# Kernel optimization log

Hardware: AMD Instinct MI355X
Metric: run time of the kernel (lower is better)

The kernel has to match this reference:

```python
import jax, jax.numpy as jnp
import numpy as np

T, B_SZ = 1024, 1024
NX, NU, ND, NM, NDT, NH = 128, 64, 32, 32, 32, 128


def setup_inputs() -> dict:
    key = jax.random.key(0)
    ks = jax.random.split(key, 10)
    return {
        "x": jax.random.normal(ks[0], (B_SZ, NX), jnp.float32),
        "M_flow": jax.random.normal(ks[1], (T, B_SZ, NM), jnp.float32),
        "DT": jax.random.normal(ks[2], (T, B_SZ, NDT), jnp.float32),
        "D": jax.random.normal(ks[3], (T, B_SZ, ND), jnp.float32),
        # ConstrainedLinear(nx, nx): weight and scalar init with torch.rand -> uniform[0,1)
        "A_weight": jax.random.uniform(ks[4], (NX, NX), jnp.float32),
        "A_scalar": jax.random.uniform(ks[5], (NX, NX), jnp.float32),
        # nn.Linear(in, out, bias=False) weights are [out, in]
        "B_w": jax.random.normal(ks[6], (NX, NU), jnp.float32) * (1.0 / np.sqrt(NU)),
        "E_w": jax.random.normal(ks[7], (NX, ND), jnp.float32) * (1.0 / np.sqrt(ND)),
        "hf1_w": jax.random.normal(ks[8], (NH, NM + NDT), jnp.float32) * (1.0 / np.sqrt(NM + NDT)),
        "hf2_w": jax.random.normal(ks[9], (NU, NH), jnp.float32) * (1.0 / np.sqrt(NH)),
    }


def reference(x, M_flow, DT, D, A_weight, A_scalar, B_w, E_w, hf1_w, hf2_w):
    # Constrained weight: ((1 - 0.1*sigmoid(scalar)) * softmax(weight, dim=1)).T
    # It is constant across time, so compute once (torch redundantly recomputes it per step).
    s_clamped = 1.0 - 0.1 * jax.nn.sigmoid(A_scalar)
    W_eff = (s_clamped * jax.nn.softmax(A_weight, axis=1)).T  # [nx, nx]

    # Per-step control input u_t depends only on exogenous M_flow/DT -> vectorize over time.
    md = jnp.concatenate([M_flow, DT], axis=2)                # [T, B, n_m+n_dT]
    h = jax.nn.relu(jnp.einsum('tbi,hi->tbh', md, hf1_w))     # [T, B, n_hidden]
    u = jax.nn.relu(jnp.einsum('tbh,uh->tbu', h, hf2_w))      # [T, B, nu]

    # Precompute additive drive B(u_t) + E(d_t); only x@W_eff is sequential.
    drive = jnp.einsum('tbu,xu->tbx', u, B_w) + jnp.einsum('tbd,xd->tbx', D, E_w)

    def step(x_prev, drive_t):
        x_new = x_prev @ W_eff + drive_t
        return x_new, x_new

    _, X = jax.lax.scan(step, x, drive)  # X: [T, B, nx]
    Y = X[:, :, -1]                      # [T, B]
    return X, Y
```

## Files before the change

### kernel.cpp

```cpp
#include <hip/hip_runtime.h>

typedef _Float16 h4 __attribute__((ext_vector_type(4)));
typedef _Float16 h8 __attribute__((ext_vector_type(8)));
typedef float f4 __attribute__((ext_vector_type(4)));

#define MFMA16(a, b, c) __builtin_amdgcn_mfma_f32_16x16x32_f16((a), (b), (c), 0, 0, 0)

static constexpr int TT  = 1024;
static constexpr int BS  = 1024;
static constexpr int LCH = 32;
static constexpr int NCH = 32;
static constexpr size_t XTOT = (size_t)TT * BS * 128;

static constexpr size_t WS_WT16 = 0;
static constexpr size_t WS_HF1  = 32768;
static constexpr size_t WS_HF2  = 49152;
static constexpr size_t WS_BW   = 65536;
static constexpr size_t WS_EW   = 81920;
static constexpr size_t WS_W32  = 90112;
static constexpr size_t WS_F    = 131072;
static constexpr size_t WS_INIT = WS_F + (size_t)NCH * BS * 128 * 4;
static constexpr size_t WS_DRV  = WS_INIT + (size_t)NCH * BS * 128 * 4;

template <typename T>
__device__ inline T ntload(const T* p) { return __builtin_nontemporal_load(p); }

__global__ void prep_kernel(const float* __restrict__ Aw, const float* __restrict__ As,
                            const float* __restrict__ hf1, const float* __restrict__ hf2,
                            const float* __restrict__ Bw, const float* __restrict__ Ew,
                            char* __restrict__ ws)
{
    const int tid = threadIdx.x;
    const int bid = blockIdx.x;
    if (bid < 128) {
        __shared__ float red[128];
        const int n = bid;
        const float a = Aw[n * 128 + tid];
        red[tid] = a;
        __syncthreads();
        for (int s = 64; s > 0; s >>= 1) {
            if (tid < s) red[tid] = fmaxf(red[tid], red[tid + s]);
            __syncthreads();
        }
        const float mx = red[0];
        __syncthreads();
        const float e = expf(a - mx);
        red[tid] = e;
        __syncthreads();
        for (int s = 64; s > 0; s >>= 1) {
            if (tid < s) red[tid] += red[tid + s];
            __syncthreads();
        }
        const float sm  = e / red[0];
        const float asv = As[n * 128 + tid];
        const float sc  = 1.0f - 0.1f * (1.0f / (1.0f + expf(-asv)));
        ((_Float16*)(ws + WS_WT16))[n * 128 + tid] = (_Float16)(sc * sm);
    } else {
        const int b2 = bid - 128;
        for (int i = b2 * 128 + tid; i < 8192; i += 32 * 128) {
            ((_Float16*)(ws + WS_HF1))[i] = (_Float16)hf1[i];
            ((_Float16*)(ws + WS_HF2))[i] = (_Float16)hf2[i];
            ((_Float16*)(ws + WS_BW))[i]  = (_Float16)Bw[i];
            if (i < 4096) ((_Float16*)(ws + WS_EW))[i] = (_Float16)Ew[i];
        }
    }
}

__global__ void w32_kernel(char* __restrict__ ws)
{
    const int tid  = threadIdx.x;
    const int lane = tid & 63;
    const int w    = tid >> 6;
    const int cl   = lane & 15;
    const int gq   = lane >> 4;

    __shared__ __align__(16) _Float16 Ta[128 * 128];
    __shared__ __align__(16) _Float16 Tb[128 * 128];

    const _Float16* Wt16 = (const _Float16*)(ws + WS_WT16);
    for (int i = tid; i < 2048; i += 256)
        *(h8*)&Ta[i * 8] = *(const h8*)&Wt16[i * 8];
    __syncthreads();

    for (int s = 0; s < 5; ++s) {
        const _Float16* src = (s & 1) ? Tb : Ta;
        _Float16* dst       = (s & 1) ? Ta : Tb;
        f4 acc[8][2];
#pragma unroll
        for (int mt = 0; mt < 8; ++mt)
#pragma unroll
            for (int nt = 0; nt < 2; ++nt) acc[mt][nt] = f4{};
#pragma unroll
        for (int kk = 0; kk < 4; ++kk) {
            h8 b0, b1;
#pragma unroll
            for (int j = 0; j < 8; ++j) {
                const int kr = kk * 32 + gq * 8 + j;
                b0[j] = src[kr * 128 + w * 32 + cl];
                b1[j] = src[kr * 128 + w * 32 + 16 + cl];
            }
#pragma unroll
            for (int mt = 0; mt < 8; ++mt) {
                h8 a = *(const h8*)&src[(mt * 16 + cl) * 128 + kk * 32 + gq * 8];
                acc[mt][0] = MFMA16(a, b0, acc[mt][0]);
                acc[mt][1] = MFMA16(a, b1, acc[mt][1]);
            }
        }
        __syncthreads();
#pragma unroll
        for (int mt = 0; mt < 8; ++mt)
#pragma unroll
            for (int nt = 0; nt < 2; ++nt)
#pragma unroll
                for (int r = 0; r < 4; ++r)
                    dst[(mt * 16 + gq * 4 + r) * 128 + w * 32 + nt * 16 + cl] =
                        (_Float16)acc[mt][nt][r];
        __syncthreads();
    }
    _Float16* W32 = (_Float16*)(ws + WS_W32);
    for (int i = tid; i < 2048; i += 256)
        *(h8*)&W32[i * 8] = *(const h8*)&Tb[i * 8];
}

__global__ __launch_bounds__(256, 4)
void drive_kernel(const float* __restrict__ Mfl, const float* __restrict__ DTi,
                  const float* __restrict__ Din, char* __restrict__ ws)
{
    const int tid  = threadIdx.x;
    const int lane = tid & 63;
    const int w    = tid >> 6;
    const int cl   = lane & 15;
    const int gq   = lane >> 4;
    const int bt   = blockIdx.x & 63;
    const int tq   = blockIdx.x >> 6;
    const int b0   = bt * 16;

    const _Float16* Hf1  = (const _Float16*)(ws + WS_HF1);
    const _Float16* Hf2  = (const _Float16*)(ws + WS_HF2);
    const _Float16* Bw16 = (const _Float16*)(ws + WS_BW);
    const _Float16* Ew16 = (const _Float16*)(ws + WS_EW);
    _Float16* Drv        = (_Float16*)(ws + WS_DRV);

    __shared__ __align__(16) _Float16 mds[4][16 * 64];
    __shared__ __align__(16) _Float16 dts[4][16 * 32];
    __shared__ __align__(16) _Float16 hs[4][16 * 128];
    __shared__ __align__(16) _Float16 us[4][16 * 64];

    const int qrow = (tid & 127) >> 3;
    const int qc4  = (tid & 7) * 4;
    f4 pm[4], pd[4];
#pragma unroll
    for (int s = 0; s < 4; ++s) {
        const size_t t  = (size_t)tq * 4 + s;
        const size_t rb = (t * BS + b0 + qrow) * 32 + qc4;
        pm[s] = (tid < 128) ? ntload((const f4*)&Mfl[rb]) : ntload((const f4*)&DTi[rb]);
        if (tid < 128) pd[s] = ntload((const f4*)&Din[rb]);
    }
#pragma unroll
    for (int s = 0; s < 4; ++s) {
        const int col = (tid < 128) ? qc4 : (32 + qc4);
        h4 hv;
#pragma unroll
        for (int j = 0; j < 4; ++j) hv[j] = (_Float16)pm[s][j];
        *(h4*)&mds[s][qrow * 64 + (((col >> 3) ^ (qrow & 7)) * 8) + (col & 7)] = hv;
        if (tid < 128) {
            h4 h2;
#pragma unroll
            for (int j = 0; j < 4; ++j) h2[j] = (_Float16)pd[s][j];
            *(h4*)&dts[s][qrow * 32 + (((qc4 >> 3) ^ (qrow & 3)) * 8) + (qc4 & 7)] = h2;
        }
    }

    h8 hf1f[2][2], bwf[2][2], ewf[2], hf2f[4];
#pragma unroll
    for (int nt = 0; nt < 2; ++nt) {
        const int ng = w * 32 + nt * 16 + cl;
#pragma unroll
        for (int kk = 0; kk < 2; ++kk) {
            hf1f[nt][kk] = *(const h8*)&Hf1[ng * 64 + kk * 32 + gq * 8];
            bwf[nt][kk]  = *(const h8*)&Bw16[ng * 64 + kk * 32 + gq * 8];
        }
        ewf[nt] = *(const h8*)&Ew16[ng * 32 + gq * 8];
    }
    {
        const int ng = w * 16 + cl;
#pragma unroll
        for (int kk = 0; kk < 4; ++kk)
            hf2f[kk] = *(const h8*)&Hf2[ng * 128 + kk * 32 + gq * 8];
    }
    __syncthreads();

#pragma unroll
    for (int s = 0; s < 4; ++s) {
        f4 ha[2] = {};
#pragma unroll
        for (int kk = 0; kk < 2; ++kk) {
            h8 a = *(const h8*)&mds[s][cl * 64 + (((kk * 4 + gq) ^ (cl & 7)) * 8)];
            ha[0] = MFMA16(a, hf1f[0][kk], ha[0]);
            ha[1] = MFMA16(a, hf1f[1][kk], ha[1]);
        }
#pragma unroll
        for (int nt = 0; nt < 2; ++nt) {
            const int colg = w * 32 + nt * 16 + cl;
#pragma unroll
            for (int r = 0; r < 4; ++r) {
                const int row = gq * 4 + r;
                hs[s][row * 128 + (((colg >> 3) ^ (row & 15)) * 8) + (colg & 7)] =
                    (_Float16)fmaxf(ha[nt][r], 0.f);
            }
        }
    }
    __syncthreads();

#pragma unroll
    for (int s = 0; s < 4; ++s) {
        f4 ua = {};
#pragma unroll
        for (int kk = 0; kk < 4; ++kk) {
            h8 a = *(const h8*)&hs[s][cl * 128 + (((kk * 4 + gq) ^ (cl & 15)) * 8)];
            ua = MFMA16(a, hf2f[kk], ua);
        }
        const int colg = w * 16 + cl;
#pragma unroll
        for (int r = 0; r < 4; ++r) {
            const int row = gq * 4 + r;
            us[s][row * 64 + (((colg >> 3) ^ (row & 7)) * 8) + (colg & 7)] =
                (_Float16)fmaxf(ua[r], 0.f);
        }
    }
    __syncthreads();

#pragma unroll
    for (int s = 0; s < 4; ++s) {
        f4 acc[2] = {};
#pragma unroll
        for (int kk = 0; kk < 2; ++kk) {
            h8 a = *(const h8*)&us[s][cl * 64 + (((kk * 4 + gq) ^ (cl & 7)) * 8)];
            acc[0] = MFMA16(a, bwf[0][kk], acc[0]);
            acc[1] = MFMA16(a, bwf[1][kk], acc[1]);
        }
        {
            h8 a = *(const h8*)&dts[s][cl * 32 + ((gq ^ (cl & 3)) * 8)];
            acc[0] = MFMA16(a, ewf[0], acc[0]);
            acc[1] = MFMA16(a, ewf[1], acc[1]);
        }
#pragma unroll
        for (int nt = 0; nt < 2; ++nt) {
            const int n = w * 32 + nt * 16 + cl;
#pragma unroll
            for (int r = 0; r < 4; ++r) {
                const int b = gq * 4 + r;
                hs[s][b * 128 + (((n >> 3) ^ b) & 15) * 8 + (n & 7)] = (_Float16)acc[nt][r];
            }
        }
    }
    __syncthreads();

    {
        const int s2 = tid >> 6;
        const int l2 = tid & 63, c2 = l2 & 15, g2 = l2 >> 4;
        const size_t t = (size_t)tq * 4 + s2;
        _Float16* dst = &Drv[(((size_t)t * 64 + bt) * 64 + l2) * 32];
#pragma unroll
        for (int p = 0; p < 4; ++p) {
            h4 lo = *(const h4*)&hs[s2][c2 * 128 + (((4 * p + (g2 >> 1)) ^ c2) & 15) * 8 + (g2 & 1) * 4];
            h4 hi = *(const h4*)&hs[s2][c2 * 128 + (((4 * p + 2 + (g2 >> 1)) ^ c2) & 15) * 8 + (g2 & 1) * 4];
            h8 o;
#pragma unroll
            for (int j = 0; j < 4; ++j) { o[j] = lo[j]; o[4 + j] = hi[j]; }
            *(h8*)&dst[p * 8] = o;
        }
    }
}

template <bool FINAL>
__global__ __launch_bounds__(256, 2)
void scan_kernel(char* __restrict__ ws,
                 float* __restrict__ Xout, float* __restrict__ Yout)
{
    const int wslot = threadIdx.x >> 6;
    const int wid   = blockIdx.x * 4 + wslot;
    const int lane  = threadIdx.x & 63;
    const int cl = lane & 15, gq = lane >> 4;
    const int c  = wid >> 6;
    const int bt = wid & 63;
    const int b0 = bt * 16;

    const _Float16* Wt16 = (const _Float16*)(ws + WS_WT16);
    const _Float16* Drv  = (const _Float16*)(ws + WS_DRV);
    float* Fbuf       = (float*)(ws + WS_F);
    const float* Init = (const float*)(ws + WS_INIT);

    __shared__ __align__(16) _Float16 tb[4][16 * 128];
    _Float16* tbuf = tb[wslot];

    h8 wf[8][4];
#pragma unroll
    for (int nt = 0; nt < 8; ++nt)
#pragma unroll
        for (int kt = 0; kt < 4; ++kt)
            wf[nt][kt] = *(const h8*)&Wt16[(nt * 16 + cl) * 128 + kt * 32 + gq * 8];

    h8 xf[4];
    if constexpr (FINAL) {
        f4 iv[8];
#pragma unroll
        for (int nt = 0; nt < 8; ++nt)
            iv[nt] = *(const f4*)&Init[((size_t)c * BS + b0 + cl) * 128 + nt * 16 + gq * 4];
#pragma unroll
        for (int nt = 0; nt < 8; ++nt) {
            h4 hv;
#pragma unroll
            for (int r = 0; r < 4; ++r) hv[r] = (_Float16)iv[nt][r];
            *(h4*)&tbuf[cl * 128 + (((nt * 2 + (gq >> 1)) ^ cl) & 15) * 8 + (gq & 1) * 4] = hv;
        }
#pragma unroll
        for (int kt = 0; kt < 4; ++kt)
            xf[kt] = *(const h8*)&tbuf[cl * 128 + (((kt * 4 + gq) ^ cl) & 15) * 8];
    } else {
#pragma unroll
        for (int kt = 0; kt < 4; ++kt) xf[kt] = h8{};
    }

    constexpr size_t STEP = 16384;
    const h8* dp = (const h8*)&Drv[(((size_t)(c * LCH) * 64 + bt) * 64 + lane) * 32];
    h8 dra0, dra1, dra2, dra3, drb0, drb1, drb2, drb3;
    dra0 = dp[0]; dra1 = dp[1]; dra2 = dp[2]; dra3 = dp[3];
    drb0 = dp[STEP + 0]; drb1 = dp[STEP + 1]; drb2 = dp[STEP + 2]; drb3 = dp[STEP + 3];

#define SCAN_STEP(K, D0, D1, D2, D3)                                                     \
    {                                                                                    \
        f4 acc[8];                                                                       \
        _Pragma("unroll") for (int r = 0; r < 4; ++r) {                                  \
            acc[0][r] = (float)D0[r]; acc[1][r] = (float)D0[4 + r];                      \
            acc[2][r] = (float)D1[r]; acc[3][r] = (float)D1[4 + r];                      \
            acc[4][r] = (float)D2[r]; acc[5][r] = (float)D2[4 + r];                      \
            acc[6][r] = (float)D3[r]; acc[7][r] = (float)D3[4 + r];                      \
        }                                                                                \
        if ((K) + 2 < LCH) {                                                             \
            D0 = dp[(size_t)((K) + 2) * STEP + 0];                                       \
            D1 = dp[(size_t)((K) + 2) * STEP + 1];                                       \
            D2 = dp[(size_t)((K) + 2) * STEP + 2];                                       \
            D3 = dp[(size_t)((K) + 2) * STEP + 3];                                       \
        }                                                                                \
        _Pragma("unroll") for (int kt = 0; kt < 4; ++kt)                                 \
            _Pragma("unroll") for (int nt = 0; nt < 8; ++nt)                             \
                acc[nt] = MFMA16(wf[nt][kt], xf[kt], acc[nt]);                           \
        if constexpr (FINAL) {                                                           \
            const size_t t = (size_t)c * LCH + (K);                                      \
            float* xp = &Xout[(t * BS + b0 + cl) * 128 + gq * 4];                        \
            _Pragma("unroll") for (int nt = 0; nt < 8; ++nt)                             \
                __builtin_nontemporal_store(acc[nt], (f4*)&xp[nt * 16]);                 \
            if (gq == 3)                                                                 \
                __builtin_nontemporal_store(acc[7][3], &Yout[t * BS + b0 + cl]);         \
        } else if ((K) == LCH - 1) {                                                     \
            _Pragma("unroll") for (int nt = 0; nt < 8; ++nt)                             \
                *(f4*)&Fbuf[((size_t)c * BS + b0 + cl) * 128 + nt * 16 + gq * 4] =       \
                    acc[nt];                                                             \
        }                                                                                \
        if ((K) < LCH - 1) {                                                             \
            _Pragma("unroll") for (int nt = 0; nt < 8; ++nt) {                           \
                h4 hv;                                                                   \
                _Pragma("unroll") for (int r = 0; r < 4; ++r)                            \
                    hv[r] = (_Float16)acc[nt][r];                                        \
                *(h4*)&tbuf[cl * 128 + (((nt * 2 + (gq >> 1)) ^ cl) & 15) * 8 +          \
                            (gq & 1) * 4] = hv;                                          \
            }                                                                            \
            _Pragma("unroll") for (int kt = 0; kt < 4; ++kt)                             \
                xf[kt] = *(const h8*)&tbuf[cl * 128 + (((kt * 4 + gq) ^ cl) & 15) * 8];  \
        }                                                                                \
    }

    for (int k = 0; k < LCH; k += 2) {
        SCAN_STEP(k, dra0, dra1, dra2, dra3);
        SCAN_STEP(k + 1, drb0, drb1, drb2, drb3);
    }
#undef SCAN_STEP
}

__global__ __launch_bounds__(64, 1)
void carry_kernel(const float* __restrict__ x0, char* __restrict__ ws, int n_steps)
{
    const int lane = threadIdx.x;
    const int cl = lane & 15, gq = lane >> 4;
    const int b0 = blockIdx.x * 16;

    const _Float16* W32 = (const _Float16*)(ws + WS_W32);
    const float* Fbuf   = (const float*)(ws + WS_F);
    float* Init         = (float*)(ws + WS_INIT);

    __shared__ __align__(16) _Float16 tbuf[16 * 128];

    h8 wf[8][4];
#pragma unroll
    for (int nt = 0; nt < 8; ++nt)
#pragma unroll
        for (int kt = 0; kt < 4; ++kt)
            wf[nt][kt] = *(const h8*)&W32[(nt * 16 + cl) * 128 + kt * 32 + gq * 8];

    h8 xf[4];
    {
        f4 iv[8];
#pragma unroll
        for (int nt = 0; nt < 8; ++nt)
            iv[nt] = *(const f4*)&x0[(size_t)(b0 + cl) * 128 + nt * 16 + gq * 4];
#pragma unroll
        for (int nt = 0; nt < 8; ++nt)
            *(f4*)&Init[(size_t)(b0 + cl) * 128 + nt * 16 + gq * 4] = iv[nt];
#pragma unroll
        for (int nt = 0; nt < 8; ++nt) {
            h4 hv;
#pragma unroll
            for (int r = 0; r < 4; ++r) hv[r] = (_Float16)iv[nt][r];
            *(h4*)&tbuf[cl * 128 + (((nt * 2 + (gq >> 1)) ^ cl) & 15) * 8 + (gq & 1) * 4] = hv;
        }
#pragma unroll
        for (int kt = 0; kt < 4; ++kt)
            xf[kt] = *(const h8*)&tbuf[cl * 128 + (((kt * 4 + gq) ^ cl) & 15) * 8];
    }

    for (int cc = 1; cc <= n_steps; ++cc) {
        f4 acc[8];
#pragma unroll
        for (int nt = 0; nt < 8; ++nt)
            acc[nt] = *(const f4*)&Fbuf[((size_t)(cc - 1) * BS + b0 + cl) * 128 + nt * 16 + gq * 4];
#pragma unroll
        for (int kt = 0; kt < 4; ++kt)
#pragma unroll
            for (int nt = 0; nt < 8; ++nt)
                acc[nt] = MFMA16(wf[nt][kt], xf[kt], acc[nt]);
#pragma unroll
        for (int nt = 0; nt < 8; ++nt)
            *(f4*)&Init[((size_t)cc * BS + b0 + cl) * 128 + nt * 16 + gq * 4] = acc[nt];
        if (cc < n_steps) {
#pragma unroll
            for (int nt = 0; nt < 8; ++nt) {
                h4 hv;
#pragma unroll
                for (int r = 0; r < 4; ++r) hv[r] = (_Float16)acc[nt][r];
                *(h4*)&tbuf[cl * 128 + (((nt * 2 + (gq >> 1)) ^ cl) & 15) * 8 + (gq & 1) * 4] = hv;
            }
#pragma unroll
            for (int kt = 0; kt < 4; ++kt)
                xf[kt] = *(const h8*)&tbuf[cl * 128 + (((kt * 4 + gq) ^ cl) & 15) * 8];
        }
    }
}

extern "C" void kernel_launch(void* const* d_in, const int* in_sizes, int n_in,
                              void* d_out, int out_size, void* d_ws, size_t ws_size,
                              hipStream_t stream)
{
    const float* x_in = (const float*)d_in[0];
    const float* Mfl  = (const float*)d_in[1];
    const float* DTi  = (const float*)d_in[2];
    const float* Din  = (const float*)d_in[3];
    const float* Aw   = (const float*)d_in[4];
    const float* As   = (const float*)d_in[5];
    const float* Bw   = (const float*)d_in[6];
    const float* Ew   = (const float*)d_in[7];
    const float* hf1  = (const float*)d_in[8];
    const float* hf2  = (const float*)d_in[9];
    char* ws    = (char*)d_ws;
    float* Xout = (float*)d_out;
    float* Yout = Xout + XTOT;

    prep_kernel<<<dim3(160), dim3(128), 0, stream>>>(Aw, As, hf1, hf2, Bw, Ew, ws);
    w32_kernel<<<dim3(1), dim3(256), 0, stream>>>(ws);

    drive_kernel<<<dim3(256 * 64), dim3(256), 0, stream>>>(Mfl, DTi, Din, ws);
    scan_kernel<false><<<dim3(496), dim3(256), 0, stream>>>(ws, nullptr, nullptr);
    carry_kernel<<<dim3(64), dim3(64), 0, stream>>>(x_in, ws, 31);
    scan_kernel<true><<<dim3(512), dim3(256), 0, stream>>>(ws, Xout, Yout);
}
```

Before: 482.8 us.

## Transpose MFMA operands in drive kernel and store drive directly in scan-fragment order

The drive-precompute kernel now swaps the MFMA A/B operands so each lane holds a row of outputs. That lets the hidden and u activations be written to LDS as packed h4 vectors instead of scalar stores. The final drive result is written straight to global memory in an interleaved layout that matches the scan kernel's fragment loads, which removes one LDS round trip and one __syncthreads. The scan kernel's drive-load addressing is changed to the new stride-64 lane-coalesced layout. Both kernels must agree on the new layout, and any mismatch would produce wrong results.

```diff
diff --git a/kernel.cpp b/kernel.cpp
--- a/kernel.cpp
+++ b/kernel.cpp
@@ -196,18 +196,16 @@
 #pragma unroll
         for (int kk = 0; kk < 2; ++kk) {
             h8 a = *(const h8*)&mds[s][cl * 64 + (((kk * 4 + gq) ^ (cl & 7)) * 8)];
-            ha[0] = MFMA16(a, hf1f[0][kk], ha[0]);
-            ha[1] = MFMA16(a, hf1f[1][kk], ha[1]);
+            ha[0] = MFMA16(hf1f[0][kk], a, ha[0]);
+            ha[1] = MFMA16(hf1f[1][kk], a, ha[1]);
         }
 #pragma unroll
         for (int nt = 0; nt < 2; ++nt) {
-            const int colg = w * 32 + nt * 16 + cl;
-#pragma unroll
-            for (int r = 0; r < 4; ++r) {
-                const int row = gq * 4 + r;
-                hs[s][row * 128 + (((colg >> 3) ^ (row & 15)) * 8) + (colg & 7)] =
-                    (_Float16)fmaxf(ha[nt][r], 0.f);
-            }
+            const int nb8 = w * 4 + nt * 2 + (gq >> 1);
+            h4 hv;
+#pragma unroll
+            for (int r = 0; r < 4; ++r) hv[r] = (_Float16)fmaxf(ha[nt][r], 0.f);
+            *(h4*)&hs[s][cl * 128 + ((nb8 ^ cl) & 15) * 8 + (gq & 1) * 4] = hv;
         }
     }
     __syncthreads();
@@ -216,17 +214,15 @@
     for (int s = 0; s < 4; ++s) {
         f4 ua = {};
 #pragma unroll
-        for (int kk = 0; kk < 4; ++kk) {
-            h8 a = *(const h8*)&hs[s][cl * 128 + (((kk * 4 + gq) ^ (cl & 15)) * 8)];
-            ua = MFMA16(a, hf2f[kk], ua);
-        }
-        const int colg = w * 16 + cl;
-#pragma unroll
-        for (int r = 0; r < 4; ++r) {
-            const int row = gq * 4 + r;
-            us[s][row * 64 + (((colg >> 3) ^ (row & 7)) * 8) + (colg & 7)] =
-                (_Float16)fmaxf(ua[r], 0.f);
-        }
+        for (int kt = 0; kt < 4; ++kt) {
+            h8 a = *(const h8*)&hs[s][cl * 128 + (((kt * 4 + gq) ^ cl) & 15) * 8];
+            ua = MFMA16(hf2f[kt], a, ua);
+        }
+        const int nb8 = w * 2 + (gq >> 1);
+        h4 hv;
+#pragma unroll
+        for (int r = 0; r < 4; ++r) hv[r] = (_Float16)fmaxf(ua[r], 0.f);
+        *(h4*)&us[s][cl * 64 + ((nb8 ^ (cl & 7)) & 7) * 8 + (gq & 1) * 4] = hv;
     }
     __syncthreads();
 
@@ -235,41 +231,20 @@
         f4 acc[2] = {};
 #pragma unroll
         for (int kk = 0; kk < 2; ++kk) {
-            h8 a = *(const h8*)&us[s][cl * 64 + (((kk * 4 + gq) ^ (cl & 7)) * 8)];
-            acc[0] = MFMA16(a, bwf[0][kk], acc[0]);
-            acc[1] = MFMA16(a, bwf[1][kk], acc[1]);
+            h8 a = *(const h8*)&us[s][cl * 64 + (((kk * 4 + gq) ^ (cl & 7)) & 7) * 8];
+            acc[0] = MFMA16(bwf[0][kk], a, acc[0]);
+            acc[1] = MFMA16(bwf[1][kk], a, acc[1]);
         }
         {
             h8 a = *(const h8*)&dts[s][cl * 32 + ((gq ^ (cl & 3)) * 8)];
-            acc[0] = MFMA16(a, ewf[0], acc[0]);
-            acc[1] = MFMA16(a, ewf[1], acc[1]);
-        }
-#pragma unroll
-        for (int nt = 0; nt < 2; ++nt) {
-            const int n = w * 32 + nt * 16 + cl;
-#pragma unroll
-            for (int r = 0; r < 4; ++r) {
-                const int b = gq * 4 + r;
-                hs[s][b * 128 + (((n >> 3) ^ b) & 15) * 8 + (n & 7)] = (_Float16)acc[nt][r];
-            }
-        }
-    }
-    __syncthreads();
-
-    {
-        const int s2 = tid >> 6;
-        const int l2 = tid & 63, c2 = l2 & 15, g2 = l2 >> 4;
-        const size_t t = (size_t)tq * 4 + s2;
-        _Float16* dst = &Drv[(((size_t)t * 64 + bt) * 64 + l2) * 32];
-#pragma unroll
-        for (int p = 0; p < 4; ++p) {
-            h4 lo = *(const h4*)&hs[s2][c2 * 128 + (((4 * p + (g2 >> 1)) ^ c2) & 15) * 8 + (g2 & 1) * 4];
-            h4 hi = *(const h4*)&hs[s2][c2 * 128 + (((4 * p + 2 + (g2 >> 1)) ^ c2) & 15) * 8 + (g2 & 1) * 4];
-            h8 o;
-#pragma unroll
-            for (int j = 0; j < 4; ++j) { o[j] = lo[j]; o[4 + j] = hi[j]; }
-            *(h8*)&dst[p * 8] = o;
-        }
+            acc[0] = MFMA16(ewf[0], a, acc[0]);
+            acc[1] = MFMA16(ewf[1], a, acc[1]);
+        }
+        h8 o;
+#pragma unroll
+        for (int r = 0; r < 4; ++r) { o[r] = (_Float16)acc[0][r]; o[4 + r] = (_Float16)acc[1][r]; }
+        const size_t t = (size_t)tq * 4 + s;
+        *(h8*)&Drv[((t * 64 + bt) * 256 + tid) * 8] = o;
     }
 }
 
@@ -323,10 +298,10 @@
     }
 
     constexpr size_t STEP = 16384;
-    const h8* dp = (const h8*)&Drv[(((size_t)(c * LCH) * 64 + bt) * 64 + lane) * 32];
+    const h8* dp = (const h8*)Drv + (((size_t)(c * LCH) * 64 + bt) * 4) * 64 + lane;
     h8 dra0, dra1, dra2, dra3, drb0, drb1, drb2, drb3;
-    dra0 = dp[0]; dra1 = dp[1]; dra2 = dp[2]; dra3 = dp[3];
-    drb0 = dp[STEP + 0]; drb1 = dp[STEP + 1]; drb2 = dp[STEP + 2]; drb3 = dp[STEP + 3];
+    dra0 = dp[0];          dra1 = dp[64];          dra2 = dp[128];          dra3 = dp[192];
+    drb0 = dp[STEP];       drb1 = dp[STEP + 64];   drb2 = dp[STEP + 128];   drb3 = dp[STEP + 192];
 
 #define SCAN_STEP(K, D0, D1, D2, D3)                                                     \
     {                                                                                    \
@@ -339,9 +314,9 @@
         }                                                                                \
         if ((K) + 2 < LCH) {                                                             \
             D0 = dp[(size_t)((K) + 2) * STEP + 0];                                       \
-            D1 = dp[(size_t)((K) + 2) * STEP + 1];                                       \
-            D2 = dp[(size_t)((K) + 2) * STEP + 2];                                       \
-            D3 = dp[(size_t)((K) + 2) * STEP + 3];                                       \
+            D1 = dp[(size_t)((K) + 2) * STEP + 64];                                      \
+            D2 = dp[(size_t)((K) + 2) * STEP + 128];                                     \
+            D3 = dp[(size_t)((K) + 2) * STEP + 192];                                     \
         }                                                                                \
         _Pragma("unroll") for (int kt = 0; kt < 4; ++kt)                                 \
             _Pragma("unroll") for (int nt = 0; nt < 8; ++nt)                             \
```

Result: faster. 456.0 us (-5.5%).
